# Kernel optimization log

Hardware: AMD Instinct MI355X
Metric: run time of the kernel (lower is better)

Reference implementation:

```python
import jax, jax.numpy as jnp
import numpy as np

IN_C = 256
OUT_C = 256
KS = 3
PAD = 1
EPS = 1e-5
BLOCK_SIZE = 256  # largest power of 2 dividing IN_C
NUM_BLOCKS = IN_C // BLOCK_SIZE


def golay_sequence(n):
    pow2 = 1
    while pow2 < n:
        pow2 *= 2
    a = np.array([1.0], dtype=np.float32)
    b = np.array([1.0], dtype=np.float32)
    while len(a) < pow2:
        a, b = np.concatenate([a, b]), np.concatenate([a, -b])
    return a[:n]


def fwht(x):
    """Unnormalized fast Walsh-Hadamard transform over the last axis (Sylvester order)."""
    base = x.shape[:-1]
    n = x.shape[-1]
    h = 1
    while h < n:
        y = x.reshape(base + (n // (2 * h), 2, h))
        a, c = y[..., 0, :], y[..., 1, :]
        x = jnp.stack([a + c, a - c], axis=-2).reshape(base + (n,))
        h *= 2
    return x


def setup_inputs() -> dict:
    key = jax.random.key(0)
    k1, k2, k3 = jax.random.split(key, 3)
    x = jax.random.normal(k1, (32, IN_C, 56, 56), dtype=jnp.float32)
    fan_in = IN_C * KS * KS
    W = jax.random.normal(k2, (OUT_C, IN_C, KS, KS), dtype=jnp.float32) / np.sqrt(fan_in)
    b = jax.random.normal(k3, (OUT_C,), dtype=jnp.float32) * 0.01
    rms_w = jnp.ones((IN_C,), dtype=jnp.float32)
    return {"x": x, "W": W, "b": b, "rms_w": rms_w}


def reference(x, W, b, rms_w):
    n, c, h, w = x.shape
    golay = jnp.asarray(golay_sequence(c)).reshape(1, c, 1, 1)
    x = x * golay                                    # Golay elementwise multiply
    x = jnp.transpose(x, (0, 2, 3, 1))               # NCHW -> NHWC
    x = x.reshape(n, h, w, NUM_BLOCKS, BLOCK_SIZE)
    x = fwht(x)                                      # blockwise Hadamard butterfly
    x = x.reshape(n, h, w, c)
    # RMSNorm over channel dim
    x = x * jax.lax.rsqrt(jnp.mean(x * x, axis=-1, keepdims=True) + EPS) * rms_w
    x = jnp.transpose(x, (0, 3, 1, 2))               # NHWC -> NCHW
    out = jax.lax.conv_general_dilated(
        x, W, window_strides=(1, 1), padding=((PAD, PAD), (PAD, PAD)),
        dimension_numbers=("NCHW", "OIHW", "NCHW"))
    return out + b[None, :, None, None]
```

## Files before the change

kernel.cpp:

```cpp
#include <hip/hip_runtime.h>
#include <hip/hip_bf16.h>

typedef short v8s __attribute__((ext_vector_type(8)));
typedef float v4f __attribute__((ext_vector_type(4)));
typedef float v16f __attribute__((ext_vector_type(16)));
typedef unsigned short u16;

#define PROW 58
#define PCOL 64

static constexpr size_t A_CC_STRIDE = (size_t)32 * PROW * PCOL * 32;
static constexpr size_t A_BYTES     = 8 * A_CC_STRIDE * 2;
static constexpr size_t WB_ELEMS    = (size_t)9 * 8 * 256 * 32;

__device__ __forceinline__ void gl2lds16(const void* gptr, void* lptr) {
  auto g = (const __attribute__((address_space(1))) unsigned int*)gptr;
  auto l = (__attribute__((address_space(3))) unsigned int*)lptr;
  __builtin_amdgcn_global_load_lds(g, l, 16, 0, 0);
}

__device__ __forceinline__ u16 f2bf(float f) {
  __hip_bfloat16 h = __float2bfloat16(f);
  union { __hip_bfloat16 b; u16 u; } cv; cv.b = h; return cv.u;
}

#define WAITVM(K) __builtin_amdgcn_s_waitcnt(0xF70 | (K))

struct alignas(16) HgTab {
  u16 v[16 * 8 * 64 * 8];
  constexpr HgTab() : v{} {
    for (int ks = 0; ks < 16; ks++)
      for (int nt = 0; nt < 8; nt++)
        for (int l = 0; l < 64; l++)
          for (int j = 0; j < 8; j++) {
            int c  = ks * 16 + ((l >> 5) << 3) + j;
            int cp = (nt << 5) + (l & 31);
            int s  = (__builtin_popcount((unsigned)(c & cp)) +
                      __builtin_popcount((unsigned)(c & (c >> 1)))) & 1;
            v[(((ks << 3) + nt) << 9) + (l << 3) + j] = (u16)(s ? 0xBF80 : 0x3F80);
          }
  }
};
static_assert(sizeof(HgTab) == 131072, "HgTab size");
__device__ const HgTab HG{};

__global__ __launch_bounds__(256, 4) void fwht_kernel(
    const float* __restrict__ x, const float* __restrict__ rms_w,
    u16* __restrict__ A)
{
  __shared__ __align__(16) float xs4[4][16][64];
  __shared__ float ssbuf[2][64];

  const int tid = threadIdx.x;
  const int y = blockIdx.x;
  const int n = blockIdx.y;

  const int lane = tid & 63;
  const int wv   = tid >> 6;
  const int mt   = wv & 1;
  const int nh   = wv >> 1;
  const int l31  = lane & 31;
  const int h    = lane >> 5;

  const int pos  = mt * 32 + l31;
  const int posl = pos > 55 ? 55 : pos;

  const float* xrow = x + (size_t)n * 802816 + (size_t)y * 56;
  const int rr4 = lane >> 4;
  int c4 = (lane & 15) * 4; if (c4 > 52) c4 = 52;

#define FSTG(KS) gl2lds16(xrow + (size_t)((KS) * 16 + wv * 4 + rr4) * 3136 + c4, \
                          &xs4[(KS) & 3][wv * 4 + rr4][(lane & 15) * 4])

  v8s bfr[2][4];
#define LOADB(KS, BK) { _Pragma("unroll") for (int nt = 0; nt < 4; nt++) \
    bfr[BK][nt] = *(const v8s*)(HG.v + ((size_t)((((KS) * 8) + nh * 4 + nt) * 64 + lane)) * 8); }

  v16f acc[4];
  #pragma unroll
  for (int nt = 0; nt < 4; nt++)
    #pragma unroll
    for (int e = 0; e < 16; e++)
      acc[nt][e] = 0.0f;

  FSTG(0);
  LOADB(0, 0)
  FSTG(1);
  FSTG(2);

#define FCOMP(S) { const float* cb = &xs4[(S) & 3][0][0]; v8s ah, al; \
    _Pragma("unroll") for (int j = 0; j < 8; j++) { \
      float v = cb[(h * 8 + j) * 64 + posl]; \
      unsigned u = __float_as_uint(v); \
      unsigned hu = u & 0xFFFF0000u; \
      float r = v - __uint_as_float(hu); \
      ah[j] = (short)(hu >> 16); \
      al[j] = (short)f2bf(r); } \
    _Pragma("unroll") for (int nt = 0; nt < 4; nt++) { \
      acc[nt] = __builtin_amdgcn_mfma_f32_32x32x16_bf16(ah, bfr[(S) & 1][nt], acc[nt], 0, 0, 0); \
      acc[nt] = __builtin_amdgcn_mfma_f32_32x32x16_bf16(al, bfr[(S) & 1][nt], acc[nt], 0, 0, 0); } }

#define FSTEP(S, KV) { \
    if ((S) < 15) LOADB((S) + 1, ((S) + 1) & 1) \
    __builtin_amdgcn_sched_barrier(0); \
    WAITVM(KV); \
    __builtin_amdgcn_sched_barrier(0); \
    __builtin_amdgcn_s_barrier(); \
    if ((S) + 3 <= 15) { FSTG((S) + 3); } \
    __builtin_amdgcn_sched_barrier(0); \
    FCOMP(S) }

  FSTEP(0, 6)  FSTEP(1, 5)  FSTEP(2, 5)  FSTEP(3, 5)
  FSTEP(4, 5)  FSTEP(5, 5)  FSTEP(6, 5)  FSTEP(7, 5)
  FSTEP(8, 5)  FSTEP(9, 5)  FSTEP(10, 5) FSTEP(11, 5)
  FSTEP(12, 5) FSTEP(13, 5) FSTEP(14, 4) FSTEP(15, 0)

  #pragma unroll
  for (int g = 0; g < 16; g++) {
    float s = acc[0][g] * acc[0][g] + acc[1][g] * acc[1][g]
            + acc[2][g] * acc[2][g] + acc[3][g] * acc[3][g];
    #pragma unroll
    for (int m = 1; m <= 16; m <<= 1) s += __shfl_xor(s, m, 64);
    if (l31 == 0)
      ssbuf[nh][mt * 32 + (g & 3) + 8 * (g >> 2) + 4 * h] = s;
  }
  __syncthreads();

  float rwv[4];
  #pragma unroll
  for (int nt = 0; nt < 4; nt++)
    rwv[nt] = rms_w[nh * 128 + nt * 32 + l31];

  const int jj  = lane & 7;
  const int icq = l31 >> 3;

  #pragma unroll
  for (int g = 0; g < 16; g++) {
    const int rg   = (g & 3) + 8 * (g >> 2) + 4 * h;
    const int posg = mt * 32 + rg;
    float ssum = ssbuf[0][posg] + ssbuf[1][posg];
    float sc = rsqrtf(ssum * (1.0f / 256.0f) + 1e-5f);
    if (posg < 56) {
      const int col = posg + 1;
      const size_t rowoff = ((size_t)icq * 64 + col) * 8 + jj;
      #pragma unroll
      for (int nt = 0; nt < 4; nt++) {
        const int cc = nh * 4 + nt;
        size_t go = (((size_t)cc * 32 + n) * PROW + (y + 1)) * 2048 + rowoff;
        A[go] = f2bf(acc[nt][g] * sc * rwv[nt]);
      }
    }
  }

  {
    const v8s z = {0,0,0,0,0,0,0,0};
    int cc = tid >> 5;
    int s  = tid & 31;
    int q  = s >> 3, cidx = s & 7;
    int col = (cidx == 0) ? 0 : (56 + cidx);
    size_t rb = (((size_t)cc * 32 + n) * PROW + (y + 1)) * 2048;
    *(v8s*)(A + rb + ((size_t)q * 64 + col) * 8) = z;
  }
  if (y == 0 || y == 55) {
    const v8s z = {0,0,0,0,0,0,0,0};
    const int r = (y == 0) ? 0 : 57;
    #pragma unroll
    for (int i = 0; i < 8; i++) {
      int c = tid + 256 * i;
      int cc = c >> 8, rem = c & 255;
      size_t go = (((size_t)cc * 32 + n) * PROW + r) * 2048 + rem * 8;
      *(v8s*)(A + go) = z;
    }
  }
#undef FSTG
#undef LOADB
#undef FCOMP
#undef FSTEP
}

__global__ __launch_bounds__(256) void wconv_kernel(
    const float* __restrict__ Wf, u16* __restrict__ Wb)
{
  int t = blockIdx.x * 256 + threadIdx.x;
  int kk = t >> 16;
  int cc = (t >> 13) & 7;
  int r  = t & 8191;
  int ocb = r >> 12;
  int q   = (r >> 10) & 3;
  int ocl = (r >> 3) & 127;
  int j   = r & 7;
  int oc = ocb * 128 + ocl;
  int ic = cc * 32 + q * 8 + j;
  int ky = kk / 3, kx = kk - ky * 3;
  float w = Wf[((oc * 256 + ic) * 3 + ky) * 3 + kx];
  Wb[t] = f2bf(w);
}

__global__ __launch_bounds__(256, 2) void conv_kernel(
    const u16* __restrict__ A, const u16* __restrict__ Wb,
    const float* __restrict__ bias, float* __restrict__ out)
{
  __shared__ __align__(16) u16 As2[2][8192];
  __shared__ __align__(16) u16 Bs2[2][12288];

  const int tid  = threadIdx.x;
  const int lane = tid & 63;
  const int wv   = tid >> 6;
  const int wm   = wv & 1;
  const int wn   = wv >> 1;
  const int m31  = lane & 31;
  const int kh8  = lane >> 5;

  const int ocb = blockIdx.x;
  const int y0  = blockIdx.y * 2;
  const int n   = blockIdx.z;

  const u16* gA = A + ((size_t)n * PROW + y0) * 2048;

  v16f acc[2][2];
  #pragma unroll
  for (int i = 0; i < 2; i++)
    #pragma unroll
    for (int j = 0; j < 2; j++)
      #pragma unroll
      for (int e = 0; e < 16; e++)
        acc[i][j][e] = 0.0f;

  int ub[2][2];
  #pragma unroll
  for (int nf = 0; nf < 2; nf++)
    #pragma unroll
    for (int kh = 0; kh < 2; kh++) {
      int ocl = wn * 64 + nf * 32 + m31;
      int q = kh * 2 + kh8;
      ub[nf][kh] = (q * 128 + ocl) * 8;
    }

#define STAGE_A(CCV) { const u16* g = gA + (size_t)(CCV) * A_CC_STRIDE + tid * 8; \
    u16* d = &As2[(CCV) & 1][0] + tid * 8; \
    _Pragma("unroll") for (int k = 0; k < 4; k++) gl2lds16(g + k * 2048, d + k * 2048); }

#define STAGE_B(CCV, KYV, BUF) { _Pragma("unroll") for (int kx = 0; kx < 3; kx++) { \
    const u16* g = Wb + ((((KYV) * 3 + kx) * 8 + (CCV)) * 8192 + ocb * 4096) + tid * 8; \
    u16* d = &Bs2[BUF][kx * 4096] + tid * 8; \
    gl2lds16(g, d); gl2lds16(g + 2048, d + 2048); } }

#define CONV_PHASE(P) { \
    if ((P) < 23) { \
      STAGE_B(((P) + 1) / 3, ((P) + 1) % 3, ((P) + 1) & 1) \
      if (((P) + 1) % 3 == 0) STAGE_A((((P) + 1) / 3) & 1 ? (((P) + 1) / 3) : (((P) + 1) / 3)) \
    } \
    __builtin_amdgcn_sched_barrier(0); \
    WAITVM((P) == 23 ? 0 : (((P) + 1) % 3 == 0 ? 10 : 6)); \
    __builtin_amdgcn_sched_barrier(0); \
    __builtin_amdgcn_s_barrier(); \
    { const u16* asb = &As2[((P) / 3) & 1][0]; \
      const u16* bsb0 = &Bs2[(P) & 1][0]; \
      _Pragma("unroll") for (int kx = 0; kx < 3; kx++) { \
        v8s af[2][2]; \
        _Pragma("unroll") for (int mf = 0; mf < 2; mf++) \
          _Pragma("unroll") for (int kh = 0; kh < 2; kh++) { \
            int col = mf * 32 + m31 + kx; \
            col = col > 63 ? 63 : col; \
            int q = kh * 2 + kh8; \
            int ua = ((wm + ((P) % 3)) * 4 + q) * 512 + col * 8; \
            af[mf][kh] = *(const v8s*)(asb + ua); } \
        v8s bf[2][2]; const u16* bsb = bsb0 + kx * 4096; \
        _Pragma("unroll") for (int nf = 0; nf < 2; nf++) \
          _Pragma("unroll") for (int kh = 0; kh < 2; kh++) \
            bf[nf][kh] = *(const v8s*)(bsb + ub[nf][kh]); \
        __builtin_amdgcn_s_setprio(1); \
        _Pragma("unroll") for (int mf = 0; mf < 2; mf++) \
          _Pragma("unroll") for (int nf = 0; nf < 2; nf++) { \
            acc[mf][nf] = __builtin_amdgcn_mfma_f32_32x32x16_bf16(af[mf][0], bf[nf][0], acc[mf][nf], 0, 0, 0); \
            acc[mf][nf] = __builtin_amdgcn_mfma_f32_32x32x16_bf16(af[mf][1], bf[nf][1], acc[mf][nf], 0, 0, 0); } \
        __builtin_amdgcn_s_setprio(0); \
      } \
    } \
    __builtin_amdgcn_s_barrier(); }

  STAGE_B(0, 0, 0)
  STAGE_A(0)

  CONV_PHASE(0)  CONV_PHASE(1)  CONV_PHASE(2)  CONV_PHASE(3)
  CONV_PHASE(4)  CONV_PHASE(5)  CONV_PHASE(6)  CONV_PHASE(7)
  CONV_PHASE(8)  CONV_PHASE(9)  CONV_PHASE(10) CONV_PHASE(11)
  CONV_PHASE(12) CONV_PHASE(13) CONV_PHASE(14) CONV_PHASE(15)
  CONV_PHASE(16) CONV_PHASE(17) CONV_PHASE(18) CONV_PHASE(19)
  CONV_PHASE(20) CONV_PHASE(21) CONV_PHASE(22) CONV_PHASE(23)

#undef STAGE_A
#undef STAGE_B
#undef CONV_PHASE

  const int yrow = y0 + wm;
  #pragma unroll
  for (int nf = 0; nf < 2; nf++) {
    const int oc = ocb * 128 + wn * 64 + nf * 32 + m31;
    const float bb = bias[oc];
    float* orow = out + ((size_t)(n * 256 + oc) * 56 + yrow) * 56;
    #pragma unroll
    for (int mf = 0; mf < 2; mf++) {
      #pragma unroll
      for (int g = 0; g < 4; g++) {
        const int x0 = mf * 32 + 8 * g + 4 * kh8;
        if (x0 < 56) {
          v4f val = { acc[mf][nf][4*g+0] + bb, acc[mf][nf][4*g+1] + bb,
                      acc[mf][nf][4*g+2] + bb, acc[mf][nf][4*g+3] + bb };
          *(v4f*)(orow + x0) = val;
        }
      }
    }
  }
}

extern "C" void kernel_launch(void* const* d_in, const int* in_sizes, int n_in,
                              void* d_out, int out_size, void* d_ws, size_t ws_size,
                              hipStream_t stream)
{
  const float* x     = (const float*)d_in[0];
  const float* Wf    = (const float*)d_in[1];
  const float* bias  = (const float*)d_in[2];
  const float* rms_w = (const float*)d_in[3];
  float* out = (float*)d_out;

  if (ws_size < A_BYTES + WB_ELEMS * 2) return;

  u16* Abf = (u16*)d_ws;
  u16* Wb  = (u16*)((char*)d_ws + A_BYTES);

  fwht_kernel<<<dim3(56, 32), 256, 0, stream>>>(x, rms_w, Abf);
  wconv_kernel<<<dim3((int)(WB_ELEMS / 256)), 256, 0, stream>>>(Wf, Wb);
  conv_kernel<<<dim3(2, 28, 32), 256, 0, stream>>>(Abf, Wb, bias, out);
}
```

Baseline: 335.2 us.

## Read conv weights directly from global memory instead of staging them in LDS

The conv kernel no longer double-buffers weight tiles in shared memory. Each wave now loads its bf16 weight fragments straight from global memory inside a per-channel-chunk loop over all nine kernel taps, and only the activation tile stays double-buffered in LDS. This cuts LDS use per block and raises the launch-bounds occupancy target from 2 to 4 blocks per CU, and it removes the per-phase weight staging and its barriers. In exchange, weight reads become exposed global/L2 loads issued by every wave, with no software prefetch hiding their latency, and the simpler waitcnt(0) plus barrier per chunk serializes the activation prefetch more coarsely.

```diff
diff --git a/kernel.cpp b/kernel.cpp
--- a/kernel.cpp
+++ b/kernel.cpp
@@ -24,7 +24,7 @@
   union { __hip_bfloat16 b; u16 u; } cv; cv.b = h; return cv.u;
 }
 
-#define WAITVM(K) __builtin_amdgcn_s_waitcnt(0xF70 | (K))
+#define WAITVM(K) asm volatile("s_waitcnt vmcnt(" #K ")" ::: "memory")
 
 struct alignas(16) HgTab {
   u16 v[16 * 8 * 64 * 8];
@@ -196,12 +196,11 @@
   Wb[t] = f2bf(w);
 }
 
-__global__ __launch_bounds__(256, 2) void conv_kernel(
+__global__ __launch_bounds__(256, 4) void conv_kernel(
     const u16* __restrict__ A, const u16* __restrict__ Wb,
     const float* __restrict__ bias, float* __restrict__ out)
 {
   __shared__ __align__(16) u16 As2[2][8192];
-  __shared__ __align__(16) u16 Bs2[2][12288];
 
   const int tid  = threadIdx.x;
   const int lane = tid & 63;
@@ -240,58 +239,39 @@
     u16* d = &As2[(CCV) & 1][0] + tid * 8; \
     _Pragma("unroll") for (int k = 0; k < 4; k++) gl2lds16(g + k * 2048, d + k * 2048); }
 
-#define STAGE_B(CCV, KYV, BUF) { _Pragma("unroll") for (int kx = 0; kx < 3; kx++) { \
-    const u16* g = Wb + ((((KYV) * 3 + kx) * 8 + (CCV)) * 8192 + ocb * 4096) + tid * 8; \
-    u16* d = &Bs2[BUF][kx * 4096] + tid * 8; \
-    gl2lds16(g, d); gl2lds16(g + 2048, d + 2048); } }
-
-#define CONV_PHASE(P) { \
-    if ((P) < 23) { \
-      STAGE_B(((P) + 1) / 3, ((P) + 1) % 3, ((P) + 1) & 1) \
-      if (((P) + 1) % 3 == 0) STAGE_A((((P) + 1) / 3) & 1 ? (((P) + 1) / 3) : (((P) + 1) / 3)) \
-    } \
+#define CONV_CC(CC) { \
+    WAITVM(0); \
+    __builtin_amdgcn_s_barrier(); \
+    if ((CC) < 7) STAGE_A((CC) + 1) \
     __builtin_amdgcn_sched_barrier(0); \
-    WAITVM((P) == 23 ? 0 : (((P) + 1) % 3 == 0 ? 10 : 6)); \
-    __builtin_amdgcn_sched_barrier(0); \
-    __builtin_amdgcn_s_barrier(); \
-    { const u16* asb = &As2[((P) / 3) & 1][0]; \
-      const u16* bsb0 = &Bs2[(P) & 1][0]; \
-      _Pragma("unroll") for (int kx = 0; kx < 3; kx++) { \
-        v8s af[2][2]; \
-        _Pragma("unroll") for (int mf = 0; mf < 2; mf++) \
-          _Pragma("unroll") for (int kh = 0; kh < 2; kh++) { \
-            int col = mf * 32 + m31 + kx; \
-            col = col > 63 ? 63 : col; \
-            int q = kh * 2 + kh8; \
-            int ua = ((wm + ((P) % 3)) * 4 + q) * 512 + col * 8; \
-            af[mf][kh] = *(const v8s*)(asb + ua); } \
-        v8s bf[2][2]; const u16* bsb = bsb0 + kx * 4096; \
-        _Pragma("unroll") for (int nf = 0; nf < 2; nf++) \
-          _Pragma("unroll") for (int kh = 0; kh < 2; kh++) \
-            bf[nf][kh] = *(const v8s*)(bsb + ub[nf][kh]); \
-        __builtin_amdgcn_s_setprio(1); \
-        _Pragma("unroll") for (int mf = 0; mf < 2; mf++) \
-          _Pragma("unroll") for (int nf = 0; nf < 2; nf++) { \
-            acc[mf][nf] = __builtin_amdgcn_mfma_f32_32x32x16_bf16(af[mf][0], bf[nf][0], acc[mf][nf], 0, 0, 0); \
-            acc[mf][nf] = __builtin_amdgcn_mfma_f32_32x32x16_bf16(af[mf][1], bf[nf][1], acc[mf][nf], 0, 0, 0); } \
-        __builtin_amdgcn_s_setprio(0); \
-      } \
-    } \
-    __builtin_amdgcn_s_barrier(); }
-
-  STAGE_B(0, 0, 0)
+    { const u16* asb = &As2[(CC) & 1][0]; \
+      _Pragma("unroll") for (int ky = 0; ky < 3; ky++) \
+        _Pragma("unroll") for (int kx = 0; kx < 3; kx++) { \
+          const u16* bt = Wb + (size_t)((((ky * 3 + kx) * 8 + (CC)) * 8192) + ocb * 4096); \
+          v8s bf[2][2]; \
+          _Pragma("unroll") for (int nf = 0; nf < 2; nf++) \
+            _Pragma("unroll") for (int kh = 0; kh < 2; kh++) \
+              bf[nf][kh] = *(const v8s*)(bt + ub[nf][kh]); \
+          v8s af[2][2]; \
+          _Pragma("unroll") for (int mf = 0; mf < 2; mf++) \
+            _Pragma("unroll") for (int kh = 0; kh < 2; kh++) { \
+              int col = mf * 32 + m31 + kx; \
+              col = col > 63 ? 63 : col; \
+              int q = kh * 2 + kh8; \
+              af[mf][kh] = *(const v8s*)(asb + ((wm + ky) * 4 + q) * 512 + col * 8); } \
+          _Pragma("unroll") for (int mf = 0; mf < 2; mf++) \
+            _Pragma("unroll") for (int nf = 0; nf < 2; nf++) { \
+              acc[mf][nf] = __builtin_amdgcn_mfma_f32_32x32x16_bf16(af[mf][0], bf[nf][0], acc[mf][nf], 0, 0, 0); \
+              acc[mf][nf] = __builtin_amdgcn_mfma_f32_32x32x16_bf16(af[mf][1], bf[nf][1], acc[mf][nf], 0, 0, 0); } \
+        } } }
+
   STAGE_A(0)
 
-  CONV_PHASE(0)  CONV_PHASE(1)  CONV_PHASE(2)  CONV_PHASE(3)
-  CONV_PHASE(4)  CONV_PHASE(5)  CONV_PHASE(6)  CONV_PHASE(7)
-  CONV_PHASE(8)  CONV_PHASE(9)  CONV_PHASE(10) CONV_PHASE(11)
-  CONV_PHASE(12) CONV_PHASE(13) CONV_PHASE(14) CONV_PHASE(15)
-  CONV_PHASE(16) CONV_PHASE(17) CONV_PHASE(18) CONV_PHASE(19)
-  CONV_PHASE(20) CONV_PHASE(21) CONV_PHASE(22) CONV_PHASE(23)
+  CONV_CC(0) CONV_CC(1) CONV_CC(2) CONV_CC(3)
+  CONV_CC(4) CONV_CC(5) CONV_CC(6) CONV_CC(7)
 
 #undef STAGE_A
-#undef STAGE_B
-#undef CONV_PHASE
+#undef CONV_CC
 
   const int yrow = y0 + wm;
   #pragma unroll
```

Measured after the change: 333.1 us. Within noise of the previous version (-0.6%).
